# Performance work log

Hardware: AMD Instinct MI355X
Metric: run time of the kernel (lower is better)

The kernel has to match this reference:

```python
import jax, jax.numpy as jnp
import numpy as np

GRID_SIZE = 5
SPLINE_ORDER = 3
COUPLING = 0.05
LN_EPS = 1e-5
BATCH = 1024
IN_DIM = 2048
HIDDEN = [4096, 4096, 2048]


def _knots():
    k = SPLINE_ORDER
    return np.concatenate([np.full(k, -1.0), np.linspace(-1.0, 1.0, GRID_SIZE + 1), np.full(k, 1.0)])


def bspline_basis(t):
    # Replicates the module's partial in-place Cox-de Boor recursion exactly:
    # after the loops, cols[0..4] are degree-3, col 5 degree-2, col 6 degree-1, col 7 degree-0.
    knots = _knots()
    k = SPLINE_ORDER
    n = len(knots) - k - 1  # 8
    cols = [jnp.where((t >= knots[i]) & (t < knots[i + 1]), 1.0, 0.0).astype(t.dtype)
            for i in range(min(n, len(knots) - 1))]
    for degree in range(1, min(k + 1, n)):
        for i in range(n - degree):
            denom1 = knots[i + degree] - knots[i]
            denom2 = knots[i + degree + 1] - knots[i + 1]
            term1 = ((t - knots[i]) / denom1) * cols[i] if denom1 > 1e-10 else 0.0
            term2 = (((knots[i + degree + 1] - t) / denom2) * cols[i + 1]
                     if (denom2 > 1e-10 and i + 1 < n) else 0.0)
            cols[i] = term1 + term2
    return jnp.stack(cols, axis=-1)  # [..., n]


def kan_activation(x, control_points, reg_weights):
    # x: [B, D]; control_points: [D, grid+order+1]; reg_weights: [D]
    t = jnp.tanh(x)
    basis = bspline_basis(t)  # [B, D, n]
    m = min(basis.shape[-1], control_points.shape[1])  # min(8, 9) = 8
    spline = jnp.einsum('bdn,dn->bd', basis[..., :m], control_points[:, :m])
    return jnp.clip(spline * reg_weights[None, :], -10.0, 10.0)


def _generators():
    sx = np.array([[0., 1.], [1., 0.]], np.float32)
    sy = np.array([[0., -1.], [1., 0.]], np.float32)
    sz = np.array([[1., 0.], [0., -1.]], np.float32)
    return np.stack([sx, sy, sz, np.eye(2, dtype=np.float32)])  # [4,2,2]

GENS = jnp.asarray(_generators())
GEN_DIAG = jnp.asarray(np.stack([np.diagonal(g) for g in _generators()]))  # [4,2]


def noncommutative_transform(x):
    # pairs of the flattened tensor, generator index cycles mod 4
    shape = x.shape
    flat = x.reshape(-1)
    P = flat.shape[0] // 2
    vec = flat[:2 * P].reshape(P, 2)
    ng = GENS.shape[0]
    if P % ng == 0:
        v = vec.reshape(P // ng, ng, 2)                      # [Q, 4, 2]
        gv = jnp.einsum('gij,qgj->qgi', GENS, v)
        vg = v * GEN_DIAG[None, :, :]
        comm = jnp.clip(gv - vg, -1.0, 1.0)
        out = (v + COUPLING * comm).reshape(-1)
    else:
        G = GENS[jnp.arange(P) % ng]
        gv = jnp.einsum('pij,pj->pi', G, vec)
        vg = vec * jnp.diagonal(G, axis1=-2, axis2=-1)
        comm = jnp.clip(gv - vg, -1.0, 1.0)
        out = (vec + COUPLING * comm).reshape(-1)
    if flat.shape[0] % 2 == 1:
        out = jnp.concatenate([out, flat[-1:]])
    return out.reshape(shape)


def setup_inputs() -> dict:
    key = jax.random.key(0)
    ks = jax.random.split(key, 16)
    inp = {'x': jax.random.normal(ks[0], (BATCH, IN_DIM), jnp.float32)}
    prev = IN_DIM
    ncp = GRID_SIZE + SPLINE_ORDER + 1  # 9
    for li, h in enumerate(HIDDEN, start=1):
        kw, kb, kc = jax.random.split(ks[li], 3)
        inp[f'W{li}'] = jax.random.normal(kw, (h, prev), jnp.float32) / np.sqrt(prev)
        inp[f'b{li}'] = jnp.zeros((h,), jnp.float32)
        inp[f'cp{li}'] = jax.random.normal(kc, (h, ncp), jnp.float32) * 0.1
        inp[f'rw{li}'] = jnp.full((h,), 0.5, jnp.float32)
        prev = h
    inp['W_out'] = jax.random.normal(ks[10], (IN_DIM, prev), jnp.float32) / np.sqrt(prev)
    inp['b_out'] = jnp.zeros((IN_DIM,), jnp.float32)
    return inp


def reference(x, W1, b1, cp1, rw1, W2, b2, cp2, rw2, W3, b3, cp3, rw3, W_out, b_out):
    # F.layer_norm over feature dim, no affine
    mu = jnp.mean(x, axis=-1, keepdims=True)
    var = jnp.var(x, axis=-1, keepdims=True)
    cur = (x - mu) / jnp.sqrt(var + LN_EPS)
    for W, b, cp, rw in ((W1, b1, cp1, rw1), (W2, b2, cp2, rw2), (W3, b3, cp3, rw3)):
        lin = cur @ W.T + b
        kan = kan_activation(lin, cp, rw)
        cur = noncommutative_transform(kan)  # dropout = identity in eval
    return cur @ W_out.T + b_out
```

## Files before the change

kernel.cpp:

```cpp
#include <hip/hip_runtime.h>

typedef __attribute__((ext_vector_type(8))) short bf16x8;
typedef __attribute__((ext_vector_type(4))) float f32x4;

__device__ __forceinline__ float b2f(unsigned short u) {
    union { unsigned int i; float f; } x; x.i = ((unsigned int)u) << 16; return x.f;
}
__device__ __forceinline__ unsigned short f2b(float f) {
    union { float f; unsigned int i; } x; x.f = f;
    unsigned int r = x.i + 0x7fffu + ((x.i >> 16) & 1u);
    return (unsigned short)(r >> 16);
}

__device__ __forceinline__ float kan_spline(float t, const float* cpf, float rwf) {
    float c3 = (t >= -1.0f && t < -0.6f) ? 1.0f : 0.0f;
    float c4 = (t >= -0.6f && t < -0.2f) ? 1.0f : 0.0f;
    float c5 = (t >= -0.2f && t <  0.2f) ? 1.0f : 0.0f;
    float c6 = (t >=  0.2f && t <  0.6f) ? 1.0f : 0.0f;
    float c7 = (t >=  0.6f && t <  1.0f) ? 1.0f : 0.0f;
    float d2 = (-0.6f - t) * 2.5f * c3;
    float d3 = (t + 1.0f) * 2.5f * c3 + (-0.2f - t) * 2.5f * c4;
    float d4 = (t + 0.6f) * 2.5f * c4 + ( 0.2f - t) * 2.5f * c5;
    float d5 = (t + 0.2f) * 2.5f * c5 + ( 0.6f - t) * 2.5f * c6;
    float d6 = (t - 0.2f) * 2.5f * c6 + ( 1.0f - t) * 2.5f * c7;
    float e1 = (-0.6f - t) * 2.5f  * d2;
    float e2 = (t + 1.0f) * 2.5f  * d2 + (-0.2f - t) * 1.25f * d3;
    float e3 = (t + 1.0f) * 1.25f * d3 + ( 0.2f - t) * 1.25f * d4;
    float e4 = (t + 0.6f) * 1.25f * d4 + ( 0.6f - t) * 1.25f * d5;
    float e5 = (t + 0.2f) * 1.25f * d5 + ( 1.0f - t) * 1.25f * d6;
    const float r12 = 1.0f / 1.2f;
    float f0 = (-0.6f - t) * 2.5f  * e1;
    float f1 = (t + 1.0f) * 2.5f  * e1 + (-0.2f - t) * 1.25f * e2;
    float f2 = (t + 1.0f) * 1.25f * e2 + ( 0.2f - t) * r12   * e3;
    float f3 = (t + 1.0f) * r12   * e3 + ( 0.6f - t) * r12   * e4;
    float f4 = (t + 0.6f) * r12   * e4 + ( 1.0f - t) * r12   * e5;
    float sp = f0*cpf[0] + f1*cpf[1] + f2*cpf[2] + f3*cpf[3] + f4*cpf[4]
             + e5*cpf[5] + d6*cpf[6] + c7*cpf[7];
    float v = sp * rwf;
    return fminf(fmaxf(v, -10.0f), 10.0f);
}

__global__ void ln_stats_kernel(const float* __restrict__ x,
                                float* __restrict__ mu, float* __restrict__ rstd) {
    const int row = blockIdx.x;
    const float* p = x + (size_t)row * 2048 + threadIdx.x * 8;
    double s = 0.0, q = 0.0;
#pragma unroll
    for (int i = 0; i < 8; ++i) { float v = p[i]; s += v; q += (double)v * v; }
    for (int o = 32; o > 0; o >>= 1) { s += __shfl_down(s, o, 64); q += __shfl_down(q, o, 64); }
    __shared__ double shs[4], shq[4];
    const int lane = threadIdx.x & 63, w = threadIdx.x >> 6;
    if (lane == 0) { shs[w] = s; shq[w] = q; }
    __syncthreads();
    if (threadIdx.x == 0) {
        double S = shs[0] + shs[1] + shs[2] + shs[3];
        double Q = shq[0] + shq[1] + shq[2] + shq[3];
        double m = S / 2048.0;
        double var = Q / 2048.0 - m * m;
        mu[row] = (float)m;
        rstd[row] = (float)(1.0 / sqrt(var + 1e-5));
    }
}

__global__ void rowsum_kernel(const float* __restrict__ W,
                              float* __restrict__ S, int K) {
    const int lane = threadIdx.x & 63, w = threadIdx.x >> 6;
    const int row = blockIdx.x * 4 + w;
    const float* p = W + (size_t)row * K;
    double s = 0.0;
    for (int c = lane * 8; c < K; c += 512) {
#pragma unroll
        for (int i = 0; i < 8; ++i) s += p[c + i];
    }
    for (int o = 32; o > 0; o >>= 1) s += __shfl_down(s, o, 64);
    if (lane == 0) S[row] = (float)s;
}

__global__ void split2_kernel(const float* __restrict__ src,
                              unsigned short* __restrict__ dst, int C) {
    const int r = blockIdx.x;
    const int c = threadIdx.x * 8;
    const float* p = src + (size_t)r * C + c;
    float4 u0 = ((const float4*)p)[0];
    float4 u1 = ((const float4*)p)[1];
    float v[8] = {u0.x, u0.y, u0.z, u0.w, u1.x, u1.y, u1.z, u1.w};
    unsigned short hi[8], lo[8];
#pragma unroll
    for (int i = 0; i < 8; ++i) {
        hi[i] = f2b(v[i]);
        lo[i] = f2b(v[i] - b2f(hi[i]));
    }
    unsigned short* d = dst + (size_t)r * 2 * C + c;
    *(uint4*)d = *(const uint4*)hi;
    *(uint4*)(d + C) = *(const uint4*)lo;
}

__global__ void cvt_kernel(const float* __restrict__ src,
                           unsigned short* __restrict__ dst) {
    const size_t i = ((size_t)blockIdx.x * 256 + threadIdx.x) * 8;
    float4 u0 = ((const float4*)(src + i))[0];
    float4 u1 = ((const float4*)(src + i))[1];
    float v[8] = {u0.x, u0.y, u0.z, u0.w, u1.x, u1.y, u1.z, u1.w};
    unsigned short t[8];
#pragma unroll
    for (int q = 0; q < 8; ++q) t[q] = f2b(v[q]);
    *(uint4*)(dst + i) = *(const uint4*)t;
}

template <int EPI, int BSRC>
__global__ __launch_bounds__(256, 2)
void gemm_kan(const void* __restrict__ Av, const void* __restrict__ Bv,
              const float* __restrict__ bias, const float* __restrict__ cp,
              const float* __restrict__ rw, const float* __restrict__ mu,
              const float* __restrict__ rstd, const float* __restrict__ S1,
              void* __restrict__ outp,
              int Nld, int n0, int Ktot, int lda, int ldb)
{
    constexpr int BM = 64, BN = 64, BK = 64, LDP = 72;
    constexpr bool SPL = (BSRC == 2);
    constexpr int OFF_B  = BM * LDP;
    constexpr int OFF_LO = (BM + BN) * LDP;
    __shared__ unsigned short lds[(SPL ? 2 : 1) * (BM + BN) * LDP];

    const int tid  = threadIdx.x;
    const int lane = tid & 63;
    const int wid  = tid >> 6;
    const int bm = blockIdx.x * BM;
    const int bn = blockIdx.y * BN;
    const int wmo = (wid >> 1) * 32;
    const int wno = (wid & 1) * 32;
    const int fr = lane & 15;
    const int kq = lane >> 4;
    const int sar = tid >> 3, sac = (tid & 7) << 3;
    const int sfr = tid >> 2, sfc = (tid & 3) << 4;

    f32x4 acc[2][2] = {};

    uint4 pA0 = {}, pA1 = {}, pB0 = {}, pB1 = {};
    const unsigned short* Ab = (const unsigned short*)Av;
    const unsigned short* Bb = (const unsigned short*)Bv;
    const size_t a0 = (size_t)(bm + sar) * lda + sac;
    const size_t a1 = (size_t)(bm + 32 + sar) * lda + sac;
    const size_t b0 = (size_t)(bn + sar) * ldb + sac;
    const size_t b1 = (size_t)(bn + 32 + sar) * ldb + sac;
    if constexpr (BSRC == 0) {
        pA0 = *(const uint4*)(Ab + a0);
        pA1 = *(const uint4*)(Ab + a1);
        pB0 = *(const uint4*)(Bb + b0);
        pB1 = *(const uint4*)(Bb + b1);
    }

    for (int k0 = 0; k0 < Ktot; k0 += BK) {
        if constexpr (BSRC == 0) {
            *(uint4*)&lds[sar * LDP + sac] = pA0;
            *(uint4*)&lds[(32 + sar) * LDP + sac] = pA1;
            *(uint4*)&lds[OFF_B + sar * LDP + sac] = pB0;
            *(uint4*)&lds[OFF_B + (32 + sar) * LDP + sac] = pB1;
        } else {
            {
                const float* g = (const float*)Bv + (size_t)(bn + sfr) * ldb + k0 + sfc;
                float4 u0 = ((const float4*)g)[0];
                float4 u1 = ((const float4*)g)[1];
                float4 u2 = ((const float4*)g)[2];
                float4 u3 = ((const float4*)g)[3];
                float v[16] = {u0.x,u0.y,u0.z,u0.w, u1.x,u1.y,u1.z,u1.w,
                               u2.x,u2.y,u2.z,u2.w, u3.x,u3.y,u3.z,u3.w};
                unsigned short hi[16], lo[16];
#pragma unroll
                for (int i = 0; i < 16; ++i) {
                    hi[i] = f2b(v[i]);
                    if (SPL) lo[i] = f2b(v[i] - b2f(hi[i]));
                }
                unsigned short* d = &lds[OFF_B + sfr * LDP + sfc];
                ((uint4*)d)[0] = *(const uint4*)&hi[0];
                ((uint4*)d)[1] = *(const uint4*)&hi[8];
                if constexpr (SPL) {
                    unsigned short* dl = d + OFF_LO;
                    ((uint4*)dl)[0] = *(const uint4*)&lo[0];
                    ((uint4*)dl)[1] = *(const uint4*)&lo[8];
                }
            }
            if constexpr (SPL) {
                const float* g = (const float*)Av + (size_t)(bm + sfr) * lda + k0 + sfc;
                float4 u0 = ((const float4*)g)[0];
                float4 u1 = ((const float4*)g)[1];
                float4 u2 = ((const float4*)g)[2];
                float4 u3 = ((const float4*)g)[3];
                float v[16] = {u0.x,u0.y,u0.z,u0.w, u1.x,u1.y,u1.z,u1.w,
                               u2.x,u2.y,u2.z,u2.w, u3.x,u3.y,u3.z,u3.w};
                unsigned short hi[16], lo[16];
#pragma unroll
                for (int i = 0; i < 16; ++i) {
                    hi[i] = f2b(v[i]);
                    lo[i] = f2b(v[i] - b2f(hi[i]));
                }
                unsigned short* d = &lds[sfr * LDP + sfc];
                ((uint4*)d)[0] = *(const uint4*)&hi[0];
                ((uint4*)d)[1] = *(const uint4*)&hi[8];
                unsigned short* dl = d + OFF_LO;
                ((uint4*)dl)[0] = *(const uint4*)&lo[0];
                ((uint4*)dl)[1] = *(const uint4*)&lo[8];
            } else {
                *(uint4*)&lds[sar * LDP + sac] = *(const uint4*)(Ab + a0 + k0);
                *(uint4*)&lds[(32 + sar) * LDP + sac] = *(const uint4*)(Ab + a1 + k0);
            }
        }
        __syncthreads();
        if constexpr (BSRC == 0) {
            if (k0 + BK < Ktot) {
                const int kn = k0 + BK;
                const int ak = (EPI == 0) ? (kn < 4096 ? kn : kn - 4096) : kn;
                const int bk = (EPI == 0) ? (kn < 2048 ? kn : kn - 2048) : kn;
                pA0 = *(const uint4*)(Ab + a0 + ak);
                pA1 = *(const uint4*)(Ab + a1 + ak);
                pB0 = *(const uint4*)(Bb + b0 + bk);
                pB1 = *(const uint4*)(Bb + b1 + bk);
            }
        }
#pragma unroll
        for (int s = 0; s < 2; ++s) {
            const int cc = (s * 4 + kq) << 3;
            bf16x8 aF[2], bF[2];
#pragma unroll
            for (int i = 0; i < 2; ++i)
                aF[i] = *(const bf16x8*)&lds[(wmo + i * 16 + fr) * LDP + cc];
#pragma unroll
            for (int j = 0; j < 2; ++j)
                bF[j] = *(const bf16x8*)&lds[OFF_B + (wno + j * 16 + fr) * LDP + cc];
#pragma unroll
            for (int i = 0; i < 2; ++i)
#pragma unroll
                for (int j = 0; j < 2; ++j)
                    acc[i][j] = __builtin_amdgcn_mfma_f32_16x16x32_bf16(aF[i], bF[j], acc[i][j], 0, 0, 0);
            if constexpr (SPL) {
                bf16x8 aL[2], bL[2];
#pragma unroll
                for (int i = 0; i < 2; ++i)
                    aL[i] = *(const bf16x8*)&lds[OFF_LO + (wmo + i * 16 + fr) * LDP + cc];
#pragma unroll
                for (int i = 0; i < 2; ++i)
#pragma unroll
                    for (int j = 0; j < 2; ++j)
                        acc[i][j] = __builtin_amdgcn_mfma_f32_16x16x32_bf16(aL[i], bF[j], acc[i][j], 0, 0, 0);
#pragma unroll
                for (int j = 0; j < 2; ++j)
                    bL[j] = *(const bf16x8*)&lds[OFF_LO + OFF_B + (wno + j * 16 + fr) * LDP + cc];
#pragma unroll
                for (int i = 0; i < 2; ++i)
#pragma unroll
                    for (int j = 0; j < 2; ++j)
                        acc[i][j] = __builtin_amdgcn_mfma_f32_16x16x32_bf16(aF[i], bL[j], acc[i][j], 0, 0, 0);
            }
        }
        __syncthreads();
    }

    const int rowg = (lane >> 4) * 4;
#pragma unroll
    for (int j = 0; j < 2; ++j) {
        const int n = n0 + bn + wno + j * 16 + fr;
        const float bs = bias[n];
        float cpf[8], rwf = 0.0f, s1 = 0.0f;
        if (EPI < 2) {
#pragma unroll
            for (int q = 0; q < 8; ++q) cpf[q] = cp[(size_t)n * 9 + q];
            rwf = rw[n];
        }
        if (EPI == 0) s1 = S1[n];
        const int s = n & 7;
#pragma unroll
        for (int i = 0; i < 2; ++i) {
            const int m0 = bm + wmo + i * 16 + rowg;
#pragma unroll
            for (int r = 0; r < 4; ++r) {
                const int m = m0 + r;
                float v = acc[i][j][r];
                if (EPI == 0) v = (v - mu[m] * s1) * rstd[m] + bs;
                else          v += bs;
                if (EPI < 2) {
                    v = kan_spline(tanhf(v), cpf, rwf);
                    float p = __shfl_xor(v, 1, 64);
                    p = fminf(fmaxf(p, -1.0f), 1.0f);
                    if (s < 4) v += ((s == 2) ? -0.05f : 0.05f) * p;
                }
                if (EPI == 2) ((float*)outp)[(size_t)m * Nld + n] = v;
                else ((unsigned short*)outp)[(size_t)m * Nld + n] = f2b(v);
            }
        }
    }
}

extern "C" void kernel_launch(void* const* d_in, const int* in_sizes, int n_in,
                              void* d_out, int out_size, void* d_ws, size_t ws_size,
                              hipStream_t stream) {
    const float* x    = (const float*)d_in[0];
    const float* W1   = (const float*)d_in[1];
    const float* b1   = (const float*)d_in[2];
    const float* cp1  = (const float*)d_in[3];
    const float* rw1  = (const float*)d_in[4];
    const float* W2   = (const float*)d_in[5];
    const float* b2   = (const float*)d_in[6];
    const float* cp2  = (const float*)d_in[7];
    const float* rw2  = (const float*)d_in[8];
    const float* W3   = (const float*)d_in[9];
    const float* b3   = (const float*)d_in[10];
    const float* cp3  = (const float*)d_in[11];
    const float* rw3  = (const float*)d_in[12];
    const float* Wout = (const float*)d_in[13];
    const float* bout = (const float*)d_in[14];

    char* ws = (char*)d_ws;
    float* mu   = (float*)(ws);
    float* rstd = (float*)(ws + 4096);
    float* S1   = (float*)(ws + 8192);
    unsigned short* A2 = (unsigned short*)(ws + 32768);
    unsigned short* A3 = (unsigned short*)(ws + 32768 + 8388608);
    unsigned short* A4 = A2;
    unsigned short* Asplit = A3;
    unsigned short* Wb = (unsigned short*)(ws + 32768 + 2 * 8388608);
    const size_t NEED_FULL = 32768 + 2 * 8388608 + 33554432;
    const size_t NEED_HALF = 32768 + 2 * 8388608 + 16777216;

    ln_stats_kernel<<<1024, 256, 0, stream>>>(x, mu, rstd);
    rowsum_kernel<<<1024, 256, 0, stream>>>(W1, S1, 2048);

    if (ws_size >= NEED_FULL) {
        split2_kernel<<<1024, 256, 0, stream>>>(x, Asplit, 2048);
        split2_kernel<<<4096, 256, 0, stream>>>(W1, Wb, 2048);
        gemm_kan<0, 0><<<dim3(16, 64), 256, 0, stream>>>(
            Asplit, Wb, b1, cp1, rw1, mu, rstd, S1, A2, 4096, 0, 6144, 4096, 4096);
        cvt_kernel<<<8192, 256, 0, stream>>>(W2, Wb);
        gemm_kan<1, 0><<<dim3(16, 64), 256, 0, stream>>>(
            A2, Wb, b2, cp2, rw2, nullptr, nullptr, nullptr, A3, 4096, 0, 4096, 4096, 4096);
        cvt_kernel<<<4096, 256, 0, stream>>>(W3, Wb);
        gemm_kan<1, 0><<<dim3(16, 32), 256, 0, stream>>>(
            A3, Wb, b3, cp3, rw3, nullptr, nullptr, nullptr, A4, 2048, 0, 4096, 4096, 4096);
        cvt_kernel<<<2048, 256, 0, stream>>>(Wout, Wb);
        gemm_kan<2, 0><<<dim3(16, 32), 256, 0, stream>>>(
            A4, Wb, bout, nullptr, nullptr, nullptr, nullptr, nullptr, d_out, 2048, 0, 2048, 2048, 2048);
    } else if (ws_size >= NEED_HALF) {
        split2_kernel<<<1024, 256, 0, stream>>>(x, Asplit, 2048);
        for (int h = 0; h < 2; ++h) {
            split2_kernel<<<2048, 256, 0, stream>>>(W1 + (size_t)h * 2048 * 2048, Wb, 2048);
            gemm_kan<0, 0><<<dim3(16, 32), 256, 0, stream>>>(
                Asplit, Wb, b1, cp1, rw1, mu, rstd, S1, A2, 4096, h * 2048, 6144, 4096, 4096);
        }
        for (int h = 0; h < 2; ++h) {
            cvt_kernel<<<4096, 256, 0, stream>>>(W2 + (size_t)h * 2048 * 4096, Wb);
            gemm_kan<1, 0><<<dim3(16, 32), 256, 0, stream>>>(
                A2, Wb, b2, cp2, rw2, nullptr, nullptr, nullptr, A3, 4096, h * 2048, 4096, 4096, 4096);
        }
        cvt_kernel<<<4096, 256, 0, stream>>>(W3, Wb);
        gemm_kan<1, 0><<<dim3(16, 32), 256, 0, stream>>>(
            A3, Wb, b3, cp3, rw3, nullptr, nullptr, nullptr, A4, 2048, 0, 4096, 4096, 4096);
        cvt_kernel<<<2048, 256, 0, stream>>>(Wout, Wb);
        gemm_kan<2, 0><<<dim3(16, 32), 256, 0, stream>>>(
            A4, Wb, bout, nullptr, nullptr, nullptr, nullptr, nullptr, d_out, 2048, 0, 2048, 2048, 2048);
    } else {
        gemm_kan<0, 2><<<dim3(16, 64), 256, 0, stream>>>(
            x, W1, b1, cp1, rw1, mu, rstd, S1, A2, 4096, 0, 2048, 2048, 2048);
        gemm_kan<1, 1><<<dim3(16, 64), 256, 0, stream>>>(
            A2, W2, b2, cp2, rw2, nullptr, nullptr, nullptr, A3, 4096, 0, 4096, 4096, 4096);
        gemm_kan<1, 1><<<dim3(16, 32), 256, 0, stream>>>(
            A3, W3, b3, cp3, rw3, nullptr, nullptr, nullptr, A4, 2048, 0, 4096, 4096, 4096);
        gemm_kan<2, 1><<<dim3(16, 32), 256, 0, stream>>>(
            A4, Wout, bout, nullptr, nullptr, nullptr, nullptr, nullptr, d_out, 2048, 0, 2048, 2048, 2048);
    }
}
```

Measured before the change: 444.7 us.

## Double-buffer LDS tiles and use 128-row tiles for the large GEMMs

The bf16 GEMM path now keeps two shared-memory tile buffers. It prefetches the next K-slice from global memory while MFMAs run on the current buffer, which removes one of the two barriers per iteration. A BM template parameter is added, and the first two layers use 128x64 tiles (each wave computes 4x2 fragments) to get more reuse per LDS load. The cost is more LDS and more registers per block, which may lower occupancy, and the larger tile halves the grid size for those layers.

```diff
diff --git a/kernel.cpp b/kernel.cpp
--- a/kernel.cpp
+++ b/kernel.cpp
@@ -107,7 +107,7 @@
     *(uint4*)(dst + i) = *(const uint4*)t;
 }
 
-template <int EPI, int BSRC>
+template <int BM, int EPI, int BSRC>
 __global__ __launch_bounds__(256, 2)
 void gemm_kan(const void* __restrict__ Av, const void* __restrict__ Bv,
               const float* __restrict__ bias, const float* __restrict__ cp,
@@ -116,47 +116,91 @@
               void* __restrict__ outp,
               int Nld, int n0, int Ktot, int lda, int ldb)
 {
-    constexpr int BM = 64, BN = 64, BK = 64, LDP = 72;
+    constexpr int BN = 64, BK = 64, LDP = 72;
+    constexpr int FM = BM / 32, FN = 2;
+    constexpr int NA = BM / 32, NB = 2;
     constexpr bool SPL = (BSRC == 2);
-    constexpr int OFF_B  = BM * LDP;
-    constexpr int OFF_LO = (BM + BN) * LDP;
-    __shared__ unsigned short lds[(SPL ? 2 : 1) * (BM + BN) * LDP];
+    constexpr int TILE  = (BM + BN) * LDP;
+    constexpr int OFFB  = BM * LDP;
+    __shared__ unsigned short lds[2 * TILE];
 
     const int tid  = threadIdx.x;
     const int lane = tid & 63;
     const int wid  = tid >> 6;
     const int bm = blockIdx.x * BM;
     const int bn = blockIdx.y * BN;
-    const int wmo = (wid >> 1) * 32;
+    const int wmo = (wid >> 1) * (BM / 2);
     const int wno = (wid & 1) * 32;
     const int fr = lane & 15;
     const int kq = lane >> 4;
-    const int sar = tid >> 3, sac = (tid & 7) << 3;
+    const int sr = tid >> 3;
+    const int sc = (tid & 7) << 3;
+    const int ldsA = sr * LDP + sc;
     const int sfr = tid >> 2, sfc = (tid & 3) << 4;
 
-    f32x4 acc[2][2] = {};
-
-    uint4 pA0 = {}, pA1 = {}, pB0 = {}, pB1 = {};
+    f32x4 acc[FM][FN] = {};
     const unsigned short* Ab = (const unsigned short*)Av;
     const unsigned short* Bb = (const unsigned short*)Bv;
-    const size_t a0 = (size_t)(bm + sar) * lda + sac;
-    const size_t a1 = (size_t)(bm + 32 + sar) * lda + sac;
-    const size_t b0 = (size_t)(bn + sar) * ldb + sac;
-    const size_t b1 = (size_t)(bn + 32 + sar) * ldb + sac;
+
+    size_t aoff[NA], boff[NB];
+#pragma unroll
+    for (int c = 0; c < NA; ++c) aoff[c] = (size_t)(bm + c * 32 + sr) * lda + sc;
+#pragma unroll
+    for (int c = 0; c < NB; ++c) boff[c] = (size_t)(bn + c * 32 + sr) * ldb + sc;
+
     if constexpr (BSRC == 0) {
-        pA0 = *(const uint4*)(Ab + a0);
-        pA1 = *(const uint4*)(Ab + a1);
-        pB0 = *(const uint4*)(Bb + b0);
-        pB1 = *(const uint4*)(Bb + b1);
-    }
-
-    for (int k0 = 0; k0 < Ktot; k0 += BK) {
-        if constexpr (BSRC == 0) {
-            *(uint4*)&lds[sar * LDP + sac] = pA0;
-            *(uint4*)&lds[(32 + sar) * LDP + sac] = pA1;
-            *(uint4*)&lds[OFF_B + sar * LDP + sac] = pB0;
-            *(uint4*)&lds[OFF_B + (32 + sar) * LDP + sac] = pB1;
-        } else {
+        uint4 pA[NA], pB[NB];
+#pragma unroll
+        for (int c = 0; c < NA; ++c) pA[c] = *(const uint4*)(Ab + aoff[c]);
+#pragma unroll
+        for (int c = 0; c < NB; ++c) pB[c] = *(const uint4*)(Bb + boff[c]);
+#pragma unroll
+        for (int c = 0; c < NA; ++c) *(uint4*)&lds[c * 32 * LDP + ldsA] = pA[c];
+#pragma unroll
+        for (int c = 0; c < NB; ++c) *(uint4*)&lds[OFFB + c * 32 * LDP + ldsA] = pB[c];
+        __syncthreads();
+
+        int cur = 0;
+        for (int k0 = 0; k0 < Ktot; k0 += BK) {
+            const bool more = (k0 + BK < Ktot);
+            if (more) {
+                const int kn = k0 + BK;
+                const int ak = (EPI == 0) ? (kn < 4096 ? kn : kn - 4096) : kn;
+                const int bk = (EPI == 0) ? (kn < 2048 ? kn : kn - 2048) : kn;
+#pragma unroll
+                for (int c = 0; c < NA; ++c) pA[c] = *(const uint4*)(Ab + aoff[c] + ak);
+#pragma unroll
+                for (int c = 0; c < NB; ++c) pB[c] = *(const uint4*)(Bb + boff[c] + bk);
+            }
+            const int B0 = cur * TILE;
+#pragma unroll
+            for (int s = 0; s < 2; ++s) {
+                const int cc = (s * 4 + kq) << 3;
+                bf16x8 aF[FM], bF[FN];
+#pragma unroll
+                for (int i = 0; i < FM; ++i)
+                    aF[i] = *(const bf16x8*)&lds[B0 + (wmo + i * 16 + fr) * LDP + cc];
+#pragma unroll
+                for (int j = 0; j < FN; ++j)
+                    bF[j] = *(const bf16x8*)&lds[B0 + OFFB + (wno + j * 16 + fr) * LDP + cc];
+#pragma unroll
+                for (int i = 0; i < FM; ++i)
+#pragma unroll
+                    for (int j = 0; j < FN; ++j)
+                        acc[i][j] = __builtin_amdgcn_mfma_f32_16x16x32_bf16(aF[i], bF[j], acc[i][j], 0, 0, 0);
+            }
+            if (more) {
+                const int B1 = (cur ^ 1) * TILE;
+#pragma unroll
+                for (int c = 0; c < NA; ++c) *(uint4*)&lds[B1 + c * 32 * LDP + ldsA] = pA[c];
+#pragma unroll
+                for (int c = 0; c < NB; ++c) *(uint4*)&lds[B1 + OFFB + c * 32 * LDP + ldsA] = pB[c];
+                __syncthreads();
+            }
+            cur ^= 1;
+        }
+    } else {
+        for (int k0 = 0; k0 < Ktot; k0 += BK) {
             {
                 const float* g = (const float*)Bv + (size_t)(bn + sfr) * ldb + k0 + sfc;
                 float4 u0 = ((const float4*)g)[0];
@@ -171,11 +215,11 @@
                     hi[i] = f2b(v[i]);
                     if (SPL) lo[i] = f2b(v[i] - b2f(hi[i]));
                 }
-                unsigned short* d = &lds[OFF_B + sfr * LDP + sfc];
+                unsigned short* d = &lds[OFFB + sfr * LDP + sfc];
                 ((uint4*)d)[0] = *(const uint4*)&hi[0];
                 ((uint4*)d)[1] = *(const uint4*)&hi[8];
                 if constexpr (SPL) {
-                    unsigned short* dl = d + OFF_LO;
+                    unsigned short* dl = d + TILE;
                     ((uint4*)dl)[0] = *(const uint4*)&lo[0];
                     ((uint4*)dl)[1] = *(const uint4*)&lo[8];
                 }
@@ -197,67 +241,57 @@
                 unsigned short* d = &lds[sfr * LDP + sfc];
                 ((uint4*)d)[0] = *(const uint4*)&hi[0];
                 ((uint4*)d)[1] = *(const uint4*)&hi[8];
-                unsigned short* dl = d + OFF_LO;
+                unsigned short* dl = d + TILE;
                 ((uint4*)dl)[0] = *(const uint4*)&lo[0];
                 ((uint4*)dl)[1] = *(const uint4*)&lo[8];
             } else {
-                *(uint4*)&lds[sar * LDP + sac] = *(const uint4*)(Ab + a0 + k0);
-                *(uint4*)&lds[(32 + sar) * LDP + sac] = *(const uint4*)(Ab + a1 + k0);
-            }
-        }
-        __syncthreads();
-        if constexpr (BSRC == 0) {
-            if (k0 + BK < Ktot) {
-                const int kn = k0 + BK;
-                const int ak = (EPI == 0) ? (kn < 4096 ? kn : kn - 4096) : kn;
-                const int bk = (EPI == 0) ? (kn < 2048 ? kn : kn - 2048) : kn;
-                pA0 = *(const uint4*)(Ab + a0 + ak);
-                pA1 = *(const uint4*)(Ab + a1 + ak);
-                pB0 = *(const uint4*)(Bb + b0 + bk);
-                pB1 = *(const uint4*)(Bb + b1 + bk);
-            }
-        }
-#pragma unroll
-        for (int s = 0; s < 2; ++s) {
-            const int cc = (s * 4 + kq) << 3;
-            bf16x8 aF[2], bF[2];
-#pragma unroll
-            for (int i = 0; i < 2; ++i)
-                aF[i] = *(const bf16x8*)&lds[(wmo + i * 16 + fr) * LDP + cc];
-#pragma unroll
-            for (int j = 0; j < 2; ++j)
-                bF[j] = *(const bf16x8*)&lds[OFF_B + (wno + j * 16 + fr) * LDP + cc];
-#pragma unroll
-            for (int i = 0; i < 2; ++i)
-#pragma unroll
-                for (int j = 0; j < 2; ++j)
-                    acc[i][j] = __builtin_amdgcn_mfma_f32_16x16x32_bf16(aF[i], bF[j], acc[i][j], 0, 0, 0);
-            if constexpr (SPL) {
-                bf16x8 aL[2], bL[2];
-#pragma unroll
-                for (int i = 0; i < 2; ++i)
-                    aL[i] = *(const bf16x8*)&lds[OFF_LO + (wmo + i * 16 + fr) * LDP + cc];
-#pragma unroll
-                for (int i = 0; i < 2; ++i)
-#pragma unroll
-                    for (int j = 0; j < 2; ++j)
-                        acc[i][j] = __builtin_amdgcn_mfma_f32_16x16x32_bf16(aL[i], bF[j], acc[i][j], 0, 0, 0);
-#pragma unroll
-                for (int j = 0; j < 2; ++j)
-                    bL[j] = *(const bf16x8*)&lds[OFF_LO + OFF_B + (wno + j * 16 + fr) * LDP + cc];
-#pragma unroll
-                for (int i = 0; i < 2; ++i)
-#pragma unroll
-                    for (int j = 0; j < 2; ++j)
-                        acc[i][j] = __builtin_amdgcn_mfma_f32_16x16x32_bf16(aF[i], bL[j], acc[i][j], 0, 0, 0);
-            }
-        }
-        __syncthreads();
+#pragma unroll
+                for (int c = 0; c < NA; ++c)
+                    *(uint4*)&lds[c * 32 * LDP + ldsA] = *(const uint4*)(Ab + aoff[c] + k0);
+            }
+            __syncthreads();
+#pragma unroll
+            for (int s = 0; s < 2; ++s) {
+                const int cc = (s * 4 + kq) << 3;
+                bf16x8 aF[FM], bF[FN];
+#pragma unroll
+                for (int i = 0; i < FM; ++i)
+                    aF[i] = *(const bf16x8*)&lds[(wmo + i * 16 + fr) * LDP + cc];
+#pragma unroll
+                for (int j = 0; j < FN; ++j)
+                    bF[j] = *(const bf16x8*)&lds[OFFB + (wno + j * 16 + fr) * LDP + cc];
+#pragma unroll
+                for (int i = 0; i < FM; ++i)
+#pragma unroll
+                    for (int j = 0; j < FN; ++j)
+                        acc[i][j] = __builtin_amdgcn_mfma_f32_16x16x32_bf16(aF[i], bF[j], acc[i][j], 0, 0, 0);
+                if constexpr (SPL) {
+                    bf16x8 aL[FM], bL[FN];
+#pragma unroll
+                    for (int i = 0; i < FM; ++i)
+                        aL[i] = *(const bf16x8*)&lds[TILE + (wmo + i * 16 + fr) * LDP + cc];
+#pragma unroll
+                    for (int i = 0; i < FM; ++i)
+#pragma unroll
+                        for (int j = 0; j < FN; ++j)
+                            acc[i][j] = __builtin_amdgcn_mfma_f32_16x16x32_bf16(aL[i], bF[j], acc[i][j], 0, 0, 0);
+#pragma unroll
+                    for (int j = 0; j < FN; ++j)
+                        bL[j] = *(const bf16x8*)&lds[TILE + OFFB + (wno + j * 16 + fr) * LDP + cc];
+#pragma unroll
+                    for (int i = 0; i < FM; ++i)
+#pragma unroll
+                        for (int j = 0; j < FN; ++j)
+                            acc[i][j] = __builtin_amdgcn_mfma_f32_16x16x32_bf16(aF[i], bL[j], acc[i][j], 0, 0, 0);
+                }
+            }
+            __syncthreads();
+        }
     }
 
     const int rowg = (lane >> 4) * 4;
 #pragma unroll
-    for (int j = 0; j < 2; ++j) {
+    for (int j = 0; j < FN; ++j) {
         const int n = n0 + bn + wno + j * 16 + fr;
         const float bs = bias[n];
         float cpf[8], rwf = 0.0f, s1 = 0.0f;
@@ -269,7 +303,7 @@
         if (EPI == 0) s1 = S1[n];
         const int s = n & 7;
 #pragma unroll
-        for (int i = 0; i < 2; ++i) {
+        for (int i = 0; i < FM; ++i) {
             const int m0 = bm + wmo + i * 16 + rowg;
 #pragma unroll
             for (int r = 0; r < 4; ++r) {
@@ -327,43 +361,43 @@
     if (ws_size >= NEED_FULL) {
         split2_kernel<<<1024, 256, 0, stream>>>(x, Asplit, 2048);
         split2_kernel<<<4096, 256, 0, stream>>>(W1, Wb, 2048);
-        gemm_kan<0, 0><<<dim3(16, 64), 256, 0, stream>>>(
+        gemm_kan<128, 0, 0><<<dim3(8, 64), 256, 0, stream>>>(
             Asplit, Wb, b1, cp1, rw1, mu, rstd, S1, A2, 4096, 0, 6144, 4096, 4096);
         cvt_kernel<<<8192, 256, 0, stream>>>(W2, Wb);
-        gemm_kan<1, 0><<<dim3(16, 64), 256, 0, stream>>>(
+        gemm_kan<128, 1, 0><<<dim3(8, 64), 256, 0, stream>>>(
             A2, Wb, b2, cp2, rw2, nullptr, nullptr, nullptr, A3, 4096, 0, 4096, 4096, 4096);
         cvt_kernel<<<4096, 256, 0, stream>>>(W3, Wb);
-        gemm_kan<1, 0><<<dim3(16, 32), 256, 0, stream>>>(
+        gemm_kan<64, 1, 0><<<dim3(16, 32), 256, 0, stream>>>(
             A3, Wb, b3, cp3, rw3, nullptr, nullptr, nullptr, A4, 2048, 0, 4096, 4096, 4096);
         cvt_kernel<<<2048, 256, 0, stream>>>(Wout, Wb);
-        gemm_kan<2, 0><<<dim3(16, 32), 256, 0, stream>>>(
+        gemm_kan<64, 2, 0><<<dim3(16, 32), 256, 0, stream>>>(
             A4, Wb, bout, nullptr, nullptr, nullptr, nullptr, nullptr, d_out, 2048, 0, 2048, 2048, 2048);
     } else if (ws_size >= NEED_HALF) {
         split2_kernel<<<1024, 256, 0, stream>>>(x, Asplit, 2048);
         for (int h = 0; h < 2; ++h) {
             split2_kernel<<<2048, 256, 0, stream>>>(W1 + (size_t)h * 2048 * 2048, Wb, 2048);
-            gemm_kan<0, 0><<<dim3(16, 32), 256, 0, stream>>>(
+            gemm_kan<128, 0, 0><<<dim3(8, 32), 256, 0, stream>>>(
                 Asplit, Wb, b1, cp1, rw1, mu, rstd, S1, A2, 4096, h * 2048, 6144, 4096, 4096);
         }
         for (int h = 0; h < 2; ++h) {
             cvt_kernel<<<4096, 256, 0, stream>>>(W2 + (size_t)h * 2048 * 4096, Wb);
-            gemm_kan<1, 0><<<dim3(16, 32), 256, 0, stream>>>(
+            gemm_kan<128, 1, 0><<<dim3(8, 32), 256, 0, stream>>>(
                 A2, Wb, b2, cp2, rw2, nullptr, nullptr, nullptr, A3, 4096, h * 2048, 4096, 4096, 4096);
         }
         cvt_kernel<<<4096, 256, 0, stream>>>(W3, Wb);
-        gemm_kan<1, 0><<<dim3(16, 32), 256, 0, stream>>>(
+        gemm_kan<64, 1, 0><<<dim3(16, 32), 256, 0, stream>>>(
             A3, Wb, b3, cp3, rw3, nullptr, nullptr, nullptr, A4, 2048, 0, 4096, 4096, 4096);
         cvt_kernel<<<2048, 256, 0, stream>>>(Wout, Wb);
-        gemm_kan<2, 0><<<dim3(16, 32), 256, 0, stream>>>(
+        gemm_kan<64, 2, 0><<<dim3(16, 32), 256, 0, stream>>>(
             A4, Wb, bout, nullptr, nullptr, nullptr, nullptr, nullptr, d_out, 2048, 0, 2048, 2048, 2048);
     } else {
-        gemm_kan<0, 2><<<dim3(16, 64), 256, 0, stream>>>(
+        gemm_kan<64, 0, 2><<<dim3(16, 64), 256, 0, stream>>>(
             x, W1, b1, cp1, rw1, mu, rstd, S1, A2, 4096, 0, 2048, 2048, 2048);
-        gemm_kan<1, 1><<<dim3(16, 64), 256, 0, stream>>>(
+        gemm_kan<64, 1, 1><<<dim3(16, 64), 256, 0, stream>>>(
             A2, W2, b2, cp2, rw2, nullptr, nullptr, nullptr, A3, 4096, 0, 4096, 4096, 4096);
-        gemm_kan<1, 1><<<dim3(16, 32), 256, 0, stream>>>(
+        gemm_kan<64, 1, 1><<<dim3(16, 32), 256, 0, stream>>>(
             A3, W3, b3, cp3, rw3, nullptr, nullptr, nullptr, A4, 2048, 0, 4096, 4096, 4096);
-        gemm_kan<2, 1><<<dim3(16, 32), 256, 0, stream>>>(
+        gemm_kan<64, 2, 1><<<dim3(16, 32), 256, 0, stream>>>(
             A4, Wout, bout, nullptr, nullptr, nullptr, nullptr, nullptr, d_out, 2048, 0, 2048, 2048, 2048);
     }
 }
```

After: 794.5 us. 1.79x slower.
